# Performance work log

Measured on AMD Instinct MI355X. Metric: run time of the kernel, lower is better.

The kernel has to match this reference:

```python
import jax, jax.numpy as jnp
import numpy as np


def mp_conv1d(x, w, groups=1, pad=0):
    # EDM2-style magnitude-preserving conv: per-out-channel unit-norm weight, no bias.
    # effective w_hat = w / (eps + ||w||/sqrt(fan_in)) / sqrt(fan_in)  ~= w / ||w||
    fan_in = w.shape[1] * w.shape[2]
    norm = jnp.sqrt(jnp.sum(jnp.square(w), axis=(1, 2), keepdims=True))
    w_hat = w / ((1e-4 + norm / np.sqrt(fan_in)) * np.sqrt(fan_in))
    return jax.lax.conv_general_dilated(
        x, w_hat, window_strides=(1,), padding=[(pad, pad)],
        dimension_numbers=('NCH', 'OIH', 'NCH'), feature_group_count=groups)


def complex_log(x, eps=1e-6):
    real = jnp.log(jnp.maximum(jnp.abs(x), eps))
    imag = (x < 0).astype(real.dtype) * np.pi
    return jax.lax.complex(real, imag)


def logcumsumexp_complex(z, axis=-1):
    # parallel prefix logcumsumexp over complex values (stabilized by real part)
    def combine(a, b):
        m = jnp.maximum(a.real, b.real)
        m_safe = jnp.where(jnp.isfinite(m), m, 0.0)  # guard (-inf,-inf) pairs
        return m_safe + jnp.log(jnp.exp(a - m_safe) + jnp.exp(b - m_safe))
    return jax.lax.associative_scan(combine, z, axis=axis)


def log_parallel_scan(log_a, log_b, log_h0):
    # heinsen associative scan: h[t] = a[t]*h[t-1] + b[t], h[-1]=h0
    log_b = jnp.concatenate([log_h0[..., None].astype(log_b.dtype), log_b], axis=-1)
    pads = [(0, 0)] * (log_a.ndim - 1) + [(1, 0)]
    a_star = jnp.pad(jnp.cumsum(log_a, axis=-1), pads)  # [... L+1]
    log_h0_plus_b_star = logcumsumexp_complex(log_b - a_star, axis=-1)
    log_h = a_star + log_h0_plus_b_star
    return jnp.exp(log_h[..., 1:]).real


def min_gru(h, g):
    # o[t] = (1-sigmoid(g[t])) * o[t-1] + sigmoid(g[t]) * h[t], h0 = 0
    log_a = jax.nn.log_sigmoid(-g)
    log_b = jax.nn.log_sigmoid(g) + complex_log(h)
    log_h0 = jnp.full(h.shape[:-1], -jnp.inf, dtype=log_b.dtype)  # log(0)
    return log_parallel_scan(log_a, log_b, log_h0).astype(h.dtype)


def setup_inputs() -> dict:
    key = jax.random.key(0)
    k1, k2, k3, k4 = jax.random.split(key, 4)
    B, D, L, O = 4, 512, 8192, 512
    return {
        'x': jax.random.normal(k1, (B, D, L), jnp.float32),
        'conv_w': jax.random.normal(k2, (D, 1, 5), jnp.float32),
        'h_w': jax.random.normal(k3, (O, D, 1), jnp.float32),
        'g_w': jax.random.normal(k4, (O - 2, D, 1), jnp.float32),
    }


def reference(x, conv_w, h_w, g_w):
    c = mp_conv1d(x, conv_w, groups=x.shape[1], pad=2)  # depthwise 5-tap
    h = mp_conv1d(c, h_w)                               # [B O L]
    g = mp_conv1d(c, g_w)                               # [B O-2 L]
    B, _, L = g.shape
    g = jnp.concatenate([
        jnp.full((B, 1, L), -1000.0, g.dtype),
        jnp.full((B, 1, L), 1000.0, g.dtype),
        g], axis=1)                                     # polarize -> [B O L]
    return min_gru(h, g)
```

## Files before the change

kernel.cpp:

```cpp
#include <hip/hip_runtime.h>
#include <hip/hip_bf16.h>
#include <math.h>

typedef float f32x4 __attribute__((ext_vector_type(4)));
typedef short s16x8 __attribute__((ext_vector_type(8)));
typedef short s16x16 __attribute__((ext_vector_type(16)));

#define B_  4
#define D_  512
#define L_  8192
#define CH_ 512
#define M_  1024

typedef const __attribute__((address_space(1))) void g_cvoid;
typedef __attribute__((address_space(3))) void lds_void;

__device__ __forceinline__ unsigned short f2bf(float f) {
    union { float f; unsigned u; } v; v.f = f;
    unsigned r = v.u + 0x7FFFu + ((v.u >> 16) & 1u);
    return (unsigned short)(r >> 16);
}

__global__ __launch_bounds__(256)
void prep_kernel(const float* __restrict__ h_w, const float* __restrict__ g_w,
                 unsigned short* __restrict__ Wn) {
    __shared__ float red[4];
    const int ch = blockIdx.x, t = threadIdx.x;
    {
        float v0 = h_w[ch * 512 + t], v1 = h_w[ch * 512 + t + 256];
        float ss = v0 * v0 + v1 * v1;
        #pragma unroll
        for (int off = 32; off > 0; off >>= 1) ss += __shfl_down(ss, off, 64);
        if ((t & 63) == 0) red[t >> 6] = ss;
        __syncthreads();
        float tot = red[0] + red[1] + red[2] + red[3];
        float scale = 1.f / (sqrtf(tot) + 1e-4f * sqrtf(512.f));
        Wn[(size_t)(2 * ch) * 512 + t]       = f2bf(v0 * scale);
        Wn[(size_t)(2 * ch) * 512 + t + 256] = f2bf(v1 * scale);
    }
    __syncthreads();
    if (ch >= 2) {
        float v0 = g_w[(ch - 2) * 512 + t], v1 = g_w[(ch - 2) * 512 + t + 256];
        float ss = v0 * v0 + v1 * v1;
        #pragma unroll
        for (int off = 32; off > 0; off >>= 1) ss += __shfl_down(ss, off, 64);
        if ((t & 63) == 0) red[t >> 6] = ss;
        __syncthreads();
        float tot = red[0] + red[1] + red[2] + red[3];
        float scale = 1.f / (sqrtf(tot) + 1e-4f * sqrtf(512.f));
        Wn[(size_t)(2 * ch + 1) * 512 + t]       = f2bf(v0 * scale);
        Wn[(size_t)(2 * ch + 1) * 512 + t + 256] = f2bf(v1 * scale);
    } else {
        Wn[(size_t)(2 * ch + 1) * 512 + t]       = 0;
        Wn[(size_t)(2 * ch + 1) * 512 + t + 256] = 0;
    }
}

__global__ __launch_bounds__(512)
void w1n_kernel(const float* __restrict__ h_w, float* __restrict__ w1n_g) {
    __shared__ float red[8];
    const int t = threadIdx.x;
    const int sg = t >> 6;
    const int lane = t & 63;
    float v = h_w[512 + t];
    float ss = v * v;
    #pragma unroll
    for (int off = 32; off > 0; off >>= 1) ss += __shfl_down(ss, off, 64);
    if (lane == 0) red[sg] = ss;
    __syncthreads();
    float tot = ((red[0] + red[1]) + (red[2] + red[3]))
              + ((red[4] + red[5]) + (red[6] + red[7]));
    float sc = 1.f / (sqrtf(tot) + 1e-4f * sqrtf(512.f));
    w1n_g[t] = v * sc;
}

__global__ __launch_bounds__(256)
void convT_kernel(const float* __restrict__ x, const float* __restrict__ cw,
                  const float* __restrict__ w1n_g,
                  unsigned short* __restrict__ CT, float* __restrict__ Pp) {
    __shared__ float xs[64][72];
    __shared__ unsigned short ct[64][72];
    __shared__ float cvf[64][65];
    const int t = threadIdx.x;
    const int l0 = blockIdx.x * 64, d0 = blockIdx.y * 64, b = blockIdx.z;
    const int r = t >> 2, q = t & 3;
    const float* xr = x + (size_t)(b * 512 + d0 + r) * L_ + (l0 - 2);
    #pragma unroll
    for (int k = 0; k < 17; ++k) {
        int c = q + 4 * k;
        int lg = l0 - 2 + c;
        xs[r][c] = (lg >= 0 && lg < L_) ? xr[c] : 0.f;
    }
    float w0 = cw[(d0 + r) * 5 + 0], w1 = cw[(d0 + r) * 5 + 1],
          w2 = cw[(d0 + r) * 5 + 2], w3 = cw[(d0 + r) * 5 + 3],
          w4 = cw[(d0 + r) * 5 + 4];
    float ss = w0 * w0 + w1 * w1 + w2 * w2 + w3 * w3 + w4 * w4;
    float scale = 1.f / (sqrtf(ss) + 1e-4f * sqrtf(5.f));
    w0 *= scale; w1 *= scale; w2 *= scale; w3 *= scale; w4 *= scale;
    __syncthreads();
    #pragma unroll
    for (int k = 0; k < 16; ++k) {
        int li = q + 4 * k;
        float acc = w0 * xs[r][li + 0] + w1 * xs[r][li + 1] + w2 * xs[r][li + 2]
                  + w3 * xs[r][li + 3] + w4 * xs[r][li + 4];
        ct[li][r] = f2bf(acc);
        cvf[li][r] = acc;
    }
    __syncthreads();
    {
        int lr = t >> 2, seg = t & 3;
        s16x16 v = *(const s16x16*)&ct[lr][seg * 16];
        *(s16x16*)&CT[(size_t)(b * 8192 + l0 + lr) * 512 + d0 + seg * 16] = v;
    }
    if (t < 64) {
        float p = 0.f;
        for (int rr = 0; rr < 64; ++rr)
            p += w1n_g[d0 + rr] * cvf[t][rr];
        Pp[((size_t)blockIdx.y * B_ + b) * L_ + l0 + t] = p;
    }
}

__global__ __launch_bounds__(256)
void fixsum_kernel(const float* __restrict__ Pp,
                   float* __restrict__ ZB, float* __restrict__ LA) {
    const int b = blockIdx.y;
    const int l = blockIdx.x * 256 + threadIdx.x;
    float acc = Pp[((size_t)0 * B_ + b) * L_ + l];
    #pragma unroll
    for (int g = 1; g < 8; ++g)
        acc += Pp[((size_t)g * B_ + b) * L_ + l];
    size_t off = ((size_t)b * CH_ + 1) * L_ + l;
    LA[off] = (acc < 0.f) ? 1000.f : -1000.f;
    ZB[off] = logf(fmaxf(fabsf(acc), 1e-6f));
}

__global__ __launch_bounds__(256)
void gemm_kernel(const unsigned short* __restrict__ Wn,
                 const unsigned short* __restrict__ CT,
                 float* __restrict__ ZB, float* __restrict__ LA) {
    __shared__ unsigned short As[128 * 64];
    __shared__ unsigned short Bs[128 * 64];
    const int t = threadIdx.x;
    const int lane = t & 63, w = t >> 6;
    const int wgid = ((blockIdx.x & 7) << 8) | (blockIdx.x >> 3);
    const int mBase = (wgid & 7) * 128;
    const int nBase = (wgid >> 3) * 128;

    const int wrow = (w >> 1) * 64, wcol = (w & 1) * 64;

    const int srow_ = lane >> 3;
    const int schk  = (lane & 7) ^ srow_;

    f32x4 acc[4][4];
    #pragma unroll
    for (int fr = 0; fr < 4; ++fr)
        #pragma unroll
        for (int fc = 0; fc < 4; ++fc)
            acc[fr][fc] = (f32x4){0.f, 0.f, 0.f, 0.f};

    const unsigned short* gA = &Wn[(size_t)(mBase + w * 32 + srow_) * 512 + schk * 8];
    const unsigned short* gB = &CT[(size_t)(nBase + w * 32 + srow_) * 512 + schk * 8];

    const int g  = lane >> 4;
    const int c0 = ((0 + g) ^ (lane & 7)) * 8;
    const int c1 = ((4 + g) ^ (lane & 7)) * 8;

    #pragma unroll
    for (int ks = 0; ks < 8; ++ks) {
        const int k0 = ks * 64;
        #pragma unroll
        for (int i = 0; i < 4; ++i) {
            __builtin_amdgcn_global_load_lds(
                (g_cvoid*)(gA + (size_t)i * 8 * 512 + k0),
                (lds_void*)&As[(w * 32 + i * 8) * 64], 16, 0, 0);
            __builtin_amdgcn_global_load_lds(
                (g_cvoid*)(gB + (size_t)i * 8 * 512 + k0),
                (lds_void*)&Bs[(w * 32 + i * 8) * 64], 16, 0, 0);
        }
        __syncthreads();
        #pragma unroll
        for (int kh = 0; kh < 2; ++kh) {
            const int cc = (kh == 0) ? c0 : c1;
            s16x8 af[4], bf[4];
            #pragma unroll
            for (int f = 0; f < 4; ++f) {
                af[f] = *(const s16x8*)&As[(wrow + f * 16 + (lane & 15)) * 64 + cc];
                bf[f] = *(const s16x8*)&Bs[(wcol + f * 16 + (lane & 15)) * 64 + cc];
            }
            #pragma unroll
            for (int fr = 0; fr < 4; ++fr)
                #pragma unroll
                for (int fc = 0; fc < 4; ++fc)
                    acc[fr][fc] = __builtin_amdgcn_mfma_f32_16x16x32_bf16(
                        af[fr], bf[fc], acc[fr][fc], 0, 0, 0);
        }
        __syncthreads();
    }

    #pragma unroll
    for (int fr = 0; fr < 4; ++fr)
    #pragma unroll
    for (int fc = 0; fc < 4; ++fc) {
        f32x4 a = acc[fr][fc];
        const int gR0 = mBase + wrow + fr * 16 + ((lane >> 4) * 4);
        const int n   = nBase + wcol + fc * 16 + (lane & 15);
        const int bb  = n >> 13, l = n & 8191;
        #pragma unroll
        for (int p = 0; p < 2; ++p) {
            float hv = a[2 * p], gv = a[2 * p + 1];
            const int ch = (gR0 >> 1) + p;
            if (ch == 0)      gv = -1000.f;
            else if (ch == 1) gv =  1000.f;
            float e  = __expf(-fabsf(gv));
            float l1 = __logf(1.f + e);
            float la = fminf(-gv, 0.f) - l1;
            float ls = fminf(gv, 0.f) - l1;
            float zb = ls + __logf(fmaxf(fabsf(hv), 1e-6f));
            float enc = (hv < 0.f) ? fabsf(la) : -fabsf(la);
            size_t off = ((size_t)bb * CH_ + ch) * L_ + l;
            ZB[off] = zb;
            LA[off] = enc;
        }
    }
}

struct LV { float re, sg; };

__device__ __forceinline__ LV lcomb(LV a, LV b) {
    float m  = fmaxf(a.re, b.re);
    float ms = (m > -3.0e38f) ? m : 0.f;
    float s  = a.sg * __expf(a.re - ms) + b.sg * __expf(b.re - ms);
    LV r;
    r.re = ms + __logf(fabsf(s));
    r.sg = (s < 0.f) ? -1.f : 1.f;
    return r;
}

__global__ __launch_bounds__(512)
void logscan_kernel(const float* __restrict__ LA, float* __restrict__ ZO) {
    __shared__ float wA[8];
    __shared__ float wRe[8], wSg[8];
    const int row = blockIdx.x;
    const int t = threadIdx.x;
    const int lane = t & 63, wid = t >> 6;
    const float* ep = LA + (size_t)row * L_;
    float* zp = ZO + (size_t)row * L_;

    float As[16];
    unsigned sgb = 0;
    float run = 0.f;
    #pragma unroll
    for (int i = 0; i < 4; ++i) {
        float4 e4 = *(const float4*)&ep[t * 16 + i * 4];
        float ev0 = e4.x, ev1 = e4.y, ev2 = e4.z, ev3 = e4.w;
        if (!(__float_as_uint(ev0) >> 31)) sgb |= (1u << (i * 4 + 0));
        if (!(__float_as_uint(ev1) >> 31)) sgb |= (1u << (i * 4 + 1));
        if (!(__float_as_uint(ev2) >> 31)) sgb |= (1u << (i * 4 + 2));
        if (!(__float_as_uint(ev3) >> 31)) sgb |= (1u << (i * 4 + 3));
        run -= fabsf(ev0); As[i * 4 + 0] = run;
        run -= fabsf(ev1); As[i * 4 + 1] = run;
        run -= fabsf(ev2); As[i * 4 + 2] = run;
        run -= fabsf(ev3); As[i * 4 + 3] = run;
    }
    float wsc = run;
    #pragma unroll
    for (int off = 1; off < 64; off <<= 1) {
        float u = __shfl_up(wsc, off, 64);
        if (lane >= off) wsc += u;
    }
    if (lane == 63) wA[wid] = wsc;
    __syncthreads();
    float pre = wsc - run;
    for (int j = 0; j < wid; ++j) pre += wA[j];
    #pragma unroll
    for (int i = 0; i < 16; ++i) As[i] += pre;

    float zz[16];
    LV tot = { -INFINITY, 1.f };
    #pragma unroll
    for (int i = 0; i < 4; ++i) {
        float4 z4 = *(const float4*)&zp[t * 16 + i * 4];
        float zv0 = z4.x, zv1 = z4.y, zv2 = z4.z, zv3 = z4.w;
        #pragma unroll
        for (int j = 0; j < 4; ++j) {
            int k = i * 4 + j;
            float zvj = (j == 0) ? zv0 : (j == 1) ? zv1 : (j == 2) ? zv2 : zv3;
            zz[k] = zvj - As[k];
            LV zi = { zz[k], ((sgb >> k) & 1) ? -1.f : 1.f };
            tot = lcomb(tot, zi);
        }
    }
    LV sc = tot;
    #pragma unroll
    for (int off = 1; off < 64; off <<= 1) {
        float ure = __shfl_up(sc.re, off, 64);
        float usg = __shfl_up(sc.sg, off, 64);
        if (lane >= off) { LV u = { ure, usg }; sc = lcomb(u, sc); }
    }
    if (lane == 63) { wRe[wid] = sc.re; wSg[wid] = sc.sg; }
    __syncthreads();
    float pr = __shfl_up(sc.re, 1, 64);
    float ps = __shfl_up(sc.sg, 1, 64);
    LV lex = { -INFINITY, 1.f };
    if (lane != 0) { lex.re = pr; lex.sg = ps; }
    LV wpre = { -INFINITY, 1.f };
    for (int j = 0; j < wid; ++j) { LV u = { wRe[j], wSg[j] }; wpre = lcomb(wpre, u); }
    LV pref = lcomb(wpre, lex);

    LV run2 = pref;
    #pragma unroll
    for (int i = 0; i < 4; ++i) {
        float4 o4;
        #pragma unroll
        for (int j = 0; j < 4; ++j) {
            int k = i * 4 + j;
            LV zi = { zz[k], ((sgb >> k) & 1) ? -1.f : 1.f };
            run2 = lcomb(run2, zi);
            float ov = run2.sg * __expf(As[k] + run2.re);
            if (j == 0) o4.x = ov; else if (j == 1) o4.y = ov;
            else if (j == 2) o4.z = ov; else o4.w = ov;
        }
        *(float4*)&zp[t * 16 + i * 4] = o4;
    }
}

extern "C" void kernel_launch(void* const* d_in, const int* in_sizes, int n_in,
                              void* d_out, int out_size, void* d_ws, size_t ws_size,
                              hipStream_t stream) {
    const float* x      = (const float*)d_in[0];
    const float* conv_w = (const float*)d_in[1];
    const float* h_w    = (const float*)d_in[2];
    const float* g_w    = (const float*)d_in[3];
    float* out = (float*)d_out;
    char* ws = (char*)d_ws;

    unsigned short* CT  = (unsigned short*)ws;
    unsigned short* Wn  = (unsigned short*)(ws + (size_t)32 * 1024 * 1024);
    float*          la  = (float*)(ws + (size_t)33 * 1024 * 1024);
    const size_t base97 = (size_t)97 * 1024 * 1024;
    float* w1n_g = (float*)(ws + base97);
    float* Pp    = (float*)(ws + base97 + 16 * 1024);

    prep_kernel<<<512, 256, 0, stream>>>(h_w, g_w, Wn);
    w1n_kernel<<<1, 512, 0, stream>>>(h_w, w1n_g);
    convT_kernel<<<dim3(128, 8, 4), 256, 0, stream>>>(x, conv_w, w1n_g, CT, Pp);
    gemm_kernel<<<2048, 256, 0, stream>>>(Wn, CT, out, la);
    fixsum_kernel<<<dim3(L_ / 256, B_), 256, 0, stream>>>(Pp, out, la);
    logscan_kernel<<<B_ * CH_, 512, 0, stream>>>(la, out);
}
```

Baseline: 146.3 us.

## Pack h/g as bf16 pairs and move log-sigmoid math into scan kernel

The GEMM epilogue now writes h and g as a packed bf16 pair per element instead of two float32 arrays of log-coefficients. The scan kernel decodes the pair and computes the log-sigmoid terms itself. The channel-1 fixup is also folded into the scan, which removes the separate fixsum launch. This halves the intermediate memory traffic, but it rounds h and g to bf16 before the nonlinear math, which can add error to the cumulative scan.

```diff
diff --git a/kernel.cpp b/kernel.cpp
--- a/kernel.cpp
+++ b/kernel.cpp
@@ -121,23 +121,9 @@
 }
 
 __global__ __launch_bounds__(256)
-void fixsum_kernel(const float* __restrict__ Pp,
-                   float* __restrict__ ZB, float* __restrict__ LA) {
-    const int b = blockIdx.y;
-    const int l = blockIdx.x * 256 + threadIdx.x;
-    float acc = Pp[((size_t)0 * B_ + b) * L_ + l];
-    #pragma unroll
-    for (int g = 1; g < 8; ++g)
-        acc += Pp[((size_t)g * B_ + b) * L_ + l];
-    size_t off = ((size_t)b * CH_ + 1) * L_ + l;
-    LA[off] = (acc < 0.f) ? 1000.f : -1000.f;
-    ZB[off] = logf(fmaxf(fabsf(acc), 1e-6f));
-}
-
-__global__ __launch_bounds__(256)
 void gemm_kernel(const unsigned short* __restrict__ Wn,
                  const unsigned short* __restrict__ CT,
-                 float* __restrict__ ZB, float* __restrict__ LA) {
+                 unsigned* __restrict__ HG) {
     __shared__ unsigned short As[128 * 64];
     __shared__ unsigned short Bs[128 * 64];
     const int t = threadIdx.x;
@@ -211,15 +197,8 @@
             const int ch = (gR0 >> 1) + p;
             if (ch == 0)      gv = -1000.f;
             else if (ch == 1) gv =  1000.f;
-            float e  = __expf(-fabsf(gv));
-            float l1 = __logf(1.f + e);
-            float la = fminf(-gv, 0.f) - l1;
-            float ls = fminf(gv, 0.f) - l1;
-            float zb = ls + __logf(fmaxf(fabsf(hv), 1e-6f));
-            float enc = (hv < 0.f) ? fabsf(la) : -fabsf(la);
             size_t off = ((size_t)bb * CH_ + ch) * L_ + l;
-            ZB[off] = zb;
-            LA[off] = enc;
+            HG[off] = ((unsigned)f2bf(hv) << 16) | (unsigned)f2bf(gv);
         }
     }
 }
@@ -237,30 +216,56 @@
 }
 
 __global__ __launch_bounds__(512)
-void logscan_kernel(const float* __restrict__ LA, float* __restrict__ ZO) {
+void logscan_kernel(const unsigned* __restrict__ HG,
+                    const float* __restrict__ Pp,
+                    float* __restrict__ Out) {
     __shared__ float wA[8];
     __shared__ float wRe[8], wSg[8];
     const int row = blockIdx.x;
     const int t = threadIdx.x;
     const int lane = t & 63, wid = t >> 6;
-    const float* ep = LA + (size_t)row * L_;
-    float* zp = ZO + (size_t)row * L_;
-
-    float As[16];
+    const bool isCh1 = ((row & 511) == 1);
+    const int bb = row >> 9;
+    const unsigned* hp = HG + (size_t)row * L_;
+    float* op = Out + (size_t)row * L_;
+
+    float As[16], zz[16];
     unsigned sgb = 0;
     float run = 0.f;
-    #pragma unroll
-    for (int i = 0; i < 4; ++i) {
-        float4 e4 = *(const float4*)&ep[t * 16 + i * 4];
-        float ev0 = e4.x, ev1 = e4.y, ev2 = e4.z, ev3 = e4.w;
-        if (!(__float_as_uint(ev0) >> 31)) sgb |= (1u << (i * 4 + 0));
-        if (!(__float_as_uint(ev1) >> 31)) sgb |= (1u << (i * 4 + 1));
-        if (!(__float_as_uint(ev2) >> 31)) sgb |= (1u << (i * 4 + 2));
-        if (!(__float_as_uint(ev3) >> 31)) sgb |= (1u << (i * 4 + 3));
-        run -= fabsf(ev0); As[i * 4 + 0] = run;
-        run -= fabsf(ev1); As[i * 4 + 1] = run;
-        run -= fabsf(ev2); As[i * 4 + 2] = run;
-        run -= fabsf(ev3); As[i * 4 + 3] = run;
+    if (isCh1) {
+        #pragma unroll
+        for (int i = 0; i < 16; ++i) {
+            const int l = t * 16 + i;
+            float acc = Pp[((size_t)0 * B_ + bb) * L_ + l];
+            #pragma unroll
+            for (int gg = 1; gg < 8; ++gg)
+                acc += Pp[((size_t)gg * B_ + bb) * L_ + l];
+            if (acc < 0.f) sgb |= (1u << i);
+            run -= 1000.f;
+            As[i] = run;
+            zz[i] = logf(fmaxf(fabsf(acc), 1e-6f));
+        }
+    } else {
+        #pragma unroll
+        for (int i = 0; i < 4; ++i) {
+            uint4 h4 = *(const uint4*)&hp[t * 16 + i * 4];
+            #pragma unroll
+            for (int j = 0; j < 4; ++j) {
+                int k = i * 4 + j;
+                unsigned w32 = (j == 0) ? h4.x : (j == 1) ? h4.y
+                             : (j == 2) ? h4.z : h4.w;
+                float hv = __uint_as_float(w32 & 0xFFFF0000u);
+                float gv = __uint_as_float(w32 << 16);
+                float e  = __expf(-fabsf(gv));
+                float l1 = __logf(1.f + e);
+                float la = fminf(-gv, 0.f) - l1;
+                float ls = fminf(gv, 0.f) - l1;
+                if (hv < 0.f) sgb |= (1u << k);
+                run += la;
+                As[k] = run;
+                zz[k] = ls + __logf(fmaxf(fabsf(hv), 1e-6f));
+            }
+        }
     }
     float wsc = run;
     #pragma unroll
@@ -275,20 +280,12 @@
     #pragma unroll
     for (int i = 0; i < 16; ++i) As[i] += pre;
 
-    float zz[16];
     LV tot = { -INFINITY, 1.f };
     #pragma unroll
-    for (int i = 0; i < 4; ++i) {
-        float4 z4 = *(const float4*)&zp[t * 16 + i * 4];
-        float zv0 = z4.x, zv1 = z4.y, zv2 = z4.z, zv3 = z4.w;
-        #pragma unroll
-        for (int j = 0; j < 4; ++j) {
-            int k = i * 4 + j;
-            float zvj = (j == 0) ? zv0 : (j == 1) ? zv1 : (j == 2) ? zv2 : zv3;
-            zz[k] = zvj - As[k];
-            LV zi = { zz[k], ((sgb >> k) & 1) ? -1.f : 1.f };
-            tot = lcomb(tot, zi);
-        }
+    for (int k = 0; k < 16; ++k) {
+        zz[k] -= As[k];
+        LV zi = { zz[k], ((sgb >> k) & 1) ? -1.f : 1.f };
+        tot = lcomb(tot, zi);
     }
     LV sc = tot;
     #pragma unroll
@@ -320,7 +317,7 @@
             if (j == 0) o4.x = ov; else if (j == 1) o4.y = ov;
             else if (j == 2) o4.z = ov; else o4.w = ov;
         }
-        *(float4*)&zp[t * 16 + i * 4] = o4;
+        *(float4*)&op[t * 16 + i * 4] = o4;
     }
 }
 
@@ -336,7 +333,7 @@
 
     unsigned short* CT  = (unsigned short*)ws;
     unsigned short* Wn  = (unsigned short*)(ws + (size_t)32 * 1024 * 1024);
-    float*          la  = (float*)(ws + (size_t)33 * 1024 * 1024);
+    unsigned*       HG  = (unsigned*)(ws + (size_t)33 * 1024 * 1024);
     const size_t base97 = (size_t)97 * 1024 * 1024;
     float* w1n_g = (float*)(ws + base97);
     float* Pp    = (float*)(ws + base97 + 16 * 1024);
@@ -344,7 +341,6 @@
     prep_kernel<<<512, 256, 0, stream>>>(h_w, g_w, Wn);
     w1n_kernel<<<1, 512, 0, stream>>>(h_w, w1n_g);
     convT_kernel<<<dim3(128, 8, 4), 256, 0, stream>>>(x, conv_w, w1n_g, CT, Pp);
-    gemm_kernel<<<2048, 256, 0, stream>>>(Wn, CT, out, la);
-    fixsum_kernel<<<dim3(L_ / 256, B_), 256, 0, stream>>>(Pp, out, la);
-    logscan_kernel<<<B_ * CH_, 512, 0, stream>>>(la, out);
-}
+    gemm_kernel<<<2048, 256, 0, stream>>>(Wn, CT, HG);
+    logscan_kernel<<<B_ * CH_, 512, 0, stream>>>(HG, Pp, out);
+}
```

Measured after the change: 149.5 us. +2.2%, slower.
